# Kernel tuning notes

Hardware: AMD Instinct MI355X
Metric: run time of the kernel (lower is better)

Reference implementation:

```python
import jax, jax.numpy as jnp
import numpy as np

EPS_MASK = 1e-9   # module fills masked scores with eps, NOT -inf
LN_EPS = 1e-5

def _layer_norm(x, g, b):
    mu = jnp.mean(x, axis=-1, keepdims=True)
    var = jnp.mean(jnp.square(x - mu), axis=-1, keepdims=True)
    return (x - mu) * jax.lax.rsqrt(var + LN_EPS) * g + b

def _mha(q_in, k_in, v_in, wq, bq, wk, bk, wv, bv, wo, bo, mask, nhead):
    B, Sq, D = q_in.shape
    dk = D // nhead
    def proj(x, w, b):
        y = x @ w + b                                   # [B,S,D]
        return y.reshape(B, -1, nhead, dk).transpose(0, 2, 1, 3)  # [B,h,S,dk]
    q, k, v = proj(q_in, wq, bq), proj(k_in, wk, bk), proj(v_in, wv, bv)
    scores = jnp.einsum('bhqd,bhkd->bhqk', q, k) / np.sqrt(dk).astype(q.dtype)
    if mask is not None:
        scores = jnp.where(mask[:, None, :, :] == 0, jnp.asarray(EPS_MASK, scores.dtype), scores)
    p = jax.nn.softmax(scores, axis=-1)                 # dropout = identity (eval)
    x = jnp.einsum('bhqk,bhkd->bhqd', p, v)
    x = x.transpose(0, 2, 1, 3).reshape(B, Sq, D)
    return x @ wo + bo

def _forward_post(tgt, memory, tgt_pos, memory_pos, tgt_mask, memory_mask, p):
    nhead = 8
    # self-attention (q=k=tgt+pos, v=tgt)
    q = tgt + tgt_pos
    sa = _mha(q, q, tgt, p['sa_wq'], p['sa_bq'], p['sa_wk'], p['sa_bk'],
              p['sa_wv'], p['sa_bv'], p['sa_wo'], p['sa_bo'], tgt_mask, nhead)
    tgt = _layer_norm(tgt + sa, p['ln1_g'], p['ln1_b'])
    # cross-attention (q=tgt+tgt_pos, k=memory+memory_pos, v=memory)
    mq = tgt + tgt_pos
    mk = memory + memory_pos
    ca = _mha(mq, mk, memory, p['ca_wq'], p['ca_bq'], p['ca_wk'], p['ca_bk'],
              p['ca_wv'], p['ca_bv'], p['ca_wo'], p['ca_bo'], memory_mask, nhead)
    tgt = _layer_norm(tgt + ca, p['ln2_g'], p['ln2_b'])
    # FFN
    h = jax.nn.relu(tgt @ p['mlp_w1'] + p['mlp_b1'])
    ff = h @ p['mlp_w2'] + p['mlp_b2']
    return _layer_norm(tgt + ff, p['ln3_g'], p['ln3_b'])

def setup_inputs() -> dict:
    key = jax.random.key(0)
    B, S, M, D, H = 4, 1024, 1024, 512, 2048
    ks = iter(jax.random.split(key, 40))
    d = {
        'tgt': jax.random.normal(next(ks), (B, S, D), jnp.float32),
        'memory': jax.random.normal(next(ks), (B, M, D), jnp.float32),
        'tgt_pos': jax.random.normal(next(ks), (B, S, D), jnp.float32),
        'memory_pos': jax.random.normal(next(ks), (B, M, D), jnp.float32),
        'tgt_mask': jax.random.randint(next(ks), (B, S, S), 0, 2, jnp.int32),
        'memory_mask': jax.random.randint(next(ks), (B, S, M), 0, 2, jnp.int32),
    }
    for pre in ('sa', 'ca'):
        for nm in ('q', 'k', 'v', 'o'):
            d[f'{pre}_w{nm}'] = jax.random.normal(next(ks), (D, D), jnp.float32) * 0.02
            d[f'{pre}_b{nm}'] = jnp.zeros((D,), jnp.float32)
    for i in (1, 2, 3):
        d[f'ln{i}_g'] = jnp.ones((D,), jnp.float32)
        d[f'ln{i}_b'] = jnp.zeros((D,), jnp.float32)
    d['mlp_w1'] = jax.random.normal(next(ks), (D, H), jnp.float32) * 0.02
    d['mlp_b1'] = jnp.zeros((H,), jnp.float32)
    d['mlp_w2'] = jax.random.normal(next(ks), (H, D), jnp.float32) * 0.02
    d['mlp_b2'] = jnp.zeros((D,), jnp.float32)
    return d

def reference(tgt, memory, tgt_pos, memory_pos, tgt_mask, memory_mask,
              sa_wq, sa_bq, sa_wk, sa_bk, sa_wv, sa_bv, sa_wo, sa_bo,
              ca_wq, ca_bq, ca_wk, ca_bk, ca_wv, ca_bv, ca_wo, ca_bo,
              ln1_g, ln1_b, ln2_g, ln2_b, ln3_g, ln3_b,
              mlp_w1, mlp_b1, mlp_w2, mlp_b2):
    p = dict(sa_wq=sa_wq, sa_bq=sa_bq, sa_wk=sa_wk, sa_bk=sa_bk, sa_wv=sa_wv,
             sa_bv=sa_bv, sa_wo=sa_wo, sa_bo=sa_bo, ca_wq=ca_wq, ca_bq=ca_bq,
             ca_wk=ca_wk, ca_bk=ca_bk, ca_wv=ca_wv, ca_bv=ca_bv, ca_wo=ca_wo,
             ca_bo=ca_bo, ln1_g=ln1_g, ln1_b=ln1_b, ln2_g=ln2_g, ln2_b=ln2_b,
             ln3_g=ln3_g, ln3_b=ln3_b, mlp_w1=mlp_w1, mlp_b1=mlp_b1,
             mlp_w2=mlp_w2, mlp_b2=mlp_b2)
    return _forward_post(tgt, memory, tgt_pos, memory_pos, tgt_mask, memory_mask, p)
```

## Files before the change

kernel.cpp:

```cpp
#include <hip/hip_runtime.h>
#include <stdint.h>

typedef unsigned int u32;
typedef unsigned long long u64;
typedef unsigned short u16;
typedef __attribute__((ext_vector_type(8))) __bf16 bf16x8;
typedef __attribute__((ext_vector_type(4))) float f32x4;

#define DEV __device__ __forceinline__

DEV u16 f2bf(float f) {
    u32 x = __builtin_bit_cast(u32, f);
    u32 r = (x + 0x7FFFu + ((x >> 16) & 1u)) >> 16;
    return (u16)r;
}

DEV float bf2f(u16 x) {
    u32 u = (u32)x << 16;
    return __builtin_bit_cast(float, u);
}

DEV bf16x8 ldg8(const u16* p) {
    return __builtin_bit_cast(bf16x8, *(const uint4*)p);
}

DEV u32 pk2(float a, float b) {
    return (u32)f2bf(a) | ((u32)f2bf(b) << 16);
}

DEV void g2l16(const u16* g, u16* l) {
    __builtin_amdgcn_global_load_lds(
        (const __attribute__((address_space(1))) u32*)g,
        (__attribute__((address_space(3))) u32*)l, 16, 0, 0);
}

DEV f32x4 mfma16(bf16x8 a, bf16x8 b, f32x4 c) {
    return __builtin_amdgcn_mfma_f32_16x16x32_bf16(a, b, c, 0, 0, 0);
}

__global__ __launch_bounds__(256) void packmask_kernel(
    const int4* __restrict__ m1, const int4* __restrict__ m2,
    u32* __restrict__ o1, u32* __restrict__ o2, int n8) {
    int i = blockIdx.x * 256 + threadIdx.x;
    bool first = i < n8;
    int idx = first ? i : i - n8;
    const int4* src = first ? m1 : m2;
    int4 a = src[idx * 2], b = src[idx * 2 + 1];
    u32 by = (u32)(a.x != 0) | ((u32)(a.y != 0) << 1) | ((u32)(a.z != 0) << 2) |
             ((u32)(a.w != 0) << 3) | ((u32)(b.x != 0) << 4) | ((u32)(b.y != 0) << 5) |
             ((u32)(b.z != 0) << 6) | ((u32)(b.w != 0) << 7);
    u32 w = by | (__shfl_down(by, 1) << 8) | (__shfl_down(by, 2) << 16) |
            (__shfl_down(by, 3) << 24);
    if ((threadIdx.x & 3) == 0) (first ? o1 : o2)[idx >> 2] = w;
}

__global__ __launch_bounds__(256) void prep_kernel(
    const float4* __restrict__ tgt, const float4* __restrict__ tpos,
    const float4* __restrict__ mem, const float4* __restrict__ mpos,
    ushort4* __restrict__ qin, ushort4* __restrict__ tgtb,
    ushort4* __restrict__ memb, ushort4* __restrict__ mkb, int n4) {
    int i = blockIdx.x * 256 + threadIdx.x;
    if (i >= n4) return;
    float4 t = tgt[i], p = tpos[i], m = mem[i], mp = mpos[i];
    qin[i]  = make_ushort4(f2bf(t.x + p.x), f2bf(t.y + p.y), f2bf(t.z + p.z), f2bf(t.w + p.w));
    tgtb[i] = make_ushort4(f2bf(t.x), f2bf(t.y), f2bf(t.z), f2bf(t.w));
    memb[i] = make_ushort4(f2bf(m.x), f2bf(m.y), f2bf(m.z), f2bf(m.w));
    mkb[i]  = make_ushort4(f2bf(m.x + mp.x), f2bf(m.y + mp.y), f2bf(m.z + mp.z), f2bf(m.w + mp.w));
}

struct W10 { const float* w[10]; };
__global__ __launch_bounds__(256) void wtrans_kernel(W10 ws, u16* wtbase) {
    int z = blockIdx.y;
    int Kd = (z == 9) ? 2048 : 512;
    int Nd = (z == 8) ? 2048 : 512;
    size_t off = (z < 8) ? (size_t)z * 262144
                         : (z == 8 ? (size_t)2097152 : (size_t)3145728);
    u16* out = wtbase + off;
    int nx = Nd / 32;
    int txile = blockIdx.x % nx, tyile = blockIdx.x / nx;
    if (tyile >= Kd / 32) return;
    const float* w = ws.w[z];
    __shared__ float t[32][33];
    int tx = threadIdx.x, ty = threadIdx.y;
#pragma unroll
    for (int j = 0; j < 4; ++j)
        t[ty + j * 8][tx] = w[(size_t)(tyile * 32 + ty + j * 8) * Nd + txile * 32 + tx];
    __syncthreads();
#pragma unroll
    for (int j = 0; j < 4; ++j)
        out[(size_t)(txile * 32 + ty + j * 8) * Kd + tyile * 32 + tx] = f2bf(t[tx][ty + j * 8]);
}

struct GemmSet { const u16* A; const u16* W; const float* bias; void* out; float oscale; int epi; };
struct GemmArgs3 { GemmSet s[3]; };

template <int BM, int BN>
__global__ __launch_bounds__(256) void gemm_kernel(GemmArgs3 args, int M, int N, int Kd) {
    constexpr int MF = BM / 32, NF = BN / 32;
    const GemmSet gs = args.s[blockIdx.z];
    const u16* __restrict__ A = gs.A;
    const u16* __restrict__ W = gs.W;
    const int t = threadIdx.x;
    const int lane = t & 63;
    const int g = lane >> 4, r16 = lane & 15;
    const int wave = t >> 6;
    const int wm = wave >> 1, wn = wave & 1;
    const int nwg = gridDim.x * gridDim.y;
    const int fid = blockIdx.y * gridDim.x + blockIdx.x;
    const int qq = nwg >> 3;
    const int lid = (fid & 7) * qq + (fid >> 3);
    const int m0 = (lid / gridDim.x) * BM, n0 = (lid % gridDim.x) * BN;

    __shared__ __align__(16) u16 As[BM * 64];
    __shared__ __align__(16) u16 Bs[BN * 64];

    f32x4 acc[MF][NF];
#pragma unroll
    for (int m = 0; m < MF; ++m)
#pragma unroll
        for (int n = 0; n < NF; ++n) acc[m][n] = f32x4{0.f, 0.f, 0.f, 0.f};

    for (int kk = 0; kk < Kd; kk += 64) {
        __syncthreads();
#pragma unroll
        for (int i = 0; i < BM / 32; ++i) {
            int cid = t + i * 256, row = cid >> 3, c = cid & 7;
            g2l16(A + (size_t)(m0 + row) * Kd + kk + ((c ^ (row & 7)) << 3), &As[cid << 3]);
        }
#pragma unroll
        for (int i = 0; i < BN / 32; ++i) {
            int cid = t + i * 256, row = cid >> 3, c = cid & 7;
            g2l16(W + (size_t)(n0 + row) * Kd + kk + ((c ^ (row & 7)) << 3), &Bs[cid << 3]);
        }
        __syncthreads();
#pragma unroll
        for (int ks = 0; ks < 2; ++ks) {
            bf16x8 af[MF], bfr[NF];
#pragma unroll
            for (int m = 0; m < MF; ++m) {
                int row = wm * (MF * 16) + m * 16 + r16;
                af[m] = *(const bf16x8*)&As[(row << 6) + (((ks * 4 + g) ^ (row & 7)) << 3)];
            }
#pragma unroll
            for (int n = 0; n < NF; ++n) {
                int row = wn * (NF * 16) + n * 16 + r16;
                bfr[n] = *(const bf16x8*)&Bs[(row << 6) + (((ks * 4 + g) ^ (row & 7)) << 3)];
            }
#pragma unroll
            for (int m = 0; m < MF; ++m)
#pragma unroll
                for (int n = 0; n < NF; ++n)
                    acc[m][n] = mfma16(af[m], bfr[n], acc[m][n]);
        }
    }
    const int epi = gs.epi;
#pragma unroll
    for (int m = 0; m < MF; ++m) {
        int row0 = m0 + wm * (MF * 16) + m * 16 + g * 4;
#pragma unroll
        for (int n = 0; n < NF; ++n) {
            int col = n0 + wn * (NF * 16) + n * 16 + r16;
            float bv = gs.bias[col];
            float v[4];
#pragma unroll
            for (int r = 0; r < 4; ++r) v[r] = (acc[m][n][r] + bv) * gs.oscale;
            if (epi == 1) {
#pragma unroll
                for (int r = 0; r < 4; ++r) v[r] = fmaxf(v[r], 0.f);
            }
            if (epi == 2) {
                float* o = (float*)gs.out;
#pragma unroll
                for (int r = 0; r < 4; ++r) o[(size_t)(row0 + r) * N + col] = v[r];
            } else if (epi == 3) {
                int bb = row0 >> 10, s = row0 & 1023;
                u16* o = (u16*)gs.out +
                         ((size_t)(bb * 8 + (col >> 6)) * 64 + (col & 63)) * 1024 + s;
                *(ushort4*)o = make_ushort4(f2bf(v[0]), f2bf(v[1]), f2bf(v[2]), f2bf(v[3]));
            } else {
                u16* o = (u16*)gs.out;
#pragma unroll
                for (int r = 0; r < 4; ++r) o[(size_t)(row0 + r) * N + col] = f2bf(v[r]);
            }
        }
    }
}

__global__ __launch_bounds__(512) void attn_part_kernel(
    const u16* __restrict__ Q, const u16* __restrict__ K,
    const u16* __restrict__ VT, const u32* __restrict__ mb,
    u16* __restrict__ OP, float2* __restrict__ ML, int Lq, int Lk) {
    const int t = threadIdx.x, lane = t & 63, wave = t >> 6;
    const int g = lane >> 4, r16 = lane & 15;
    const int h = blockIdx.y;
    const int b = blockIdx.z >> 2, p = blockIdx.z & 3;
    const int bh = b * 8 + h;
    const int q0 = blockIdx.x * 128 + wave * 16;
    const int kc0 = p * (Lk >> 2);
    const int NCH = (Lk >> 2) >> 5;

    __shared__ __align__(16) u16 Ks[2][32][64];
    __shared__ __align__(16) u16 Vs[2][64][32];
    __shared__ __align__(16) u16 Pl[8][16][40];

    const size_t qrow = (size_t)b * Lq + q0 + r16;
    const u16* qp = Q + qrow * 512 + h * 64 + g * 8;
    bf16x8 qb0 = ldg8(qp), qb1 = ldg8(qp + 32);
    const u32* mrow = mb + qrow * (Lk >> 5);

    const int sid = t & 255;
    const bool isK = t < 256;
    const int srow = sid >> 3, sc = sid & 7;
    const int vd = sid >> 2, vc = sid & 3;
    const u16* sg = isK
        ? K + (size_t)b * Lk * 512 + h * 64 + (size_t)srow * 512 + ((sc ^ (srow & 7)) << 3)
        : VT + ((size_t)bh * 64 + vd) * Lk + (vc << 3);
    u16* const sl = (isK ? &Ks[0][0][0] : &Vs[0][0][0]) + sid * 8;
    const size_t sstride = isK ? 512 : 1;

    f32x4 acc[4];
#pragma unroll
    for (int dt = 0; dt < 4; ++dt) acc[dt] = f32x4{0.f, 0.f, 0.f, 0.f};
    float mrun = -INFINITY, lrun = 0.f;
    const f32x4 zf = {0.f, 0.f, 0.f, 0.f};

    g2l16(sg + (size_t)kc0 * sstride, sl);
    __syncthreads();

    for (int c = 0; c < NCH; ++c) {
        const int buf = c & 1, nbuf = buf ^ 1;
        const int kc = kc0 + c * 32;
        if (c + 1 < NCH)
            g2l16(sg + (size_t)(kc + 32) * sstride, sl + nbuf * 2048);
        const u16* kb = &Ks[buf][0][0];
        const u16* vb = &Vs[buf][0][0];
        const int r1 = 16 + r16;
        bf16x8 k00 = *(const bf16x8*)(kb + r16 * 64 + ((g ^ (r16 & 7)) << 3));
        bf16x8 k01 = *(const bf16x8*)(kb + r16 * 64 + (((4 + g) ^ (r16 & 7)) << 3));
        bf16x8 k10 = *(const bf16x8*)(kb + r1 * 64 + ((g ^ (r16 & 7)) << 3));
        bf16x8 k11 = *(const bf16x8*)(kb + r1 * 64 + (((4 + g) ^ (r16 & 7)) << 3));
        f32x4 s0 = mfma16(k00, qb0, zf); s0 = mfma16(k01, qb1, s0);
        f32x4 s1 = mfma16(k10, qb0, zf); s1 = mfma16(k11, qb1, s1);

        u32 mw = mrow[kc >> 5];
        float sv[8];
#pragma unroll
        for (int r = 0; r < 4; ++r) {
            sv[r]     = ((mw >> (g * 4 + r)) & 1) ? s0[r] : 1e-9f;
            sv[4 + r] = ((mw >> (16 + g * 4 + r)) & 1) ? s1[r] : 1e-9f;
        }
        float tm = fmaxf(fmaxf(fmaxf(sv[0], sv[1]), fmaxf(sv[2], sv[3])),
                         fmaxf(fmaxf(sv[4], sv[5]), fmaxf(sv[6], sv[7])));
        tm = fmaxf(tm, __shfl_xor(tm, 16));
        tm = fmaxf(tm, __shfl_xor(tm, 32));
        if (!__all(tm <= mrun + 8.f)) {
            float mn = fmaxf(mrun, tm);
            float alpha = __expf(mrun - mn);
            mrun = mn;
            lrun *= alpha;
#pragma unroll
            for (int r = 0; r < 4; ++r) {
                float ar = __shfl(alpha, g * 4 + r);
#pragma unroll
                for (int dt = 0; dt < 4; ++dt) acc[dt][r] *= ar;
            }
        }
        float ts = 0.f;
#pragma unroll
        for (int j = 0; j < 8; ++j) { sv[j] = __expf(sv[j] - mrun); ts += sv[j]; }
        ts += __shfl_xor(ts, 16);
        ts += __shfl_xor(ts, 32);
        lrun += ts;

        uint2 u0; u0.x = pk2(sv[0], sv[1]); u0.y = pk2(sv[2], sv[3]);
        uint2 u1; u1.x = pk2(sv[4], sv[5]); u1.y = pk2(sv[6], sv[7]);
        *(uint2*)&Pl[wave][r16][g * 4] = u0;
        *(uint2*)&Pl[wave][r16][16 + g * 4] = u1;
        bf16x8 pf = *(const bf16x8*)&Pl[wave][r16][g * 8];
#pragma unroll
        for (int dt = 0; dt < 4; ++dt) {
            bf16x8 vf = *(const bf16x8*)(vb + (dt * 16 + r16) * 32 + g * 8);
            acc[dt] = mfma16(pf, vf, acc[dt]);
        }
        __syncthreads();
    }

    if (lane < 16)
        ML[(size_t)p * 32768 + (size_t)bh * 1024 + q0 + lane] = make_float2(mrun, lrun);
    const size_t obase = (size_t)p * 2097152 + ((size_t)bh * 1024 + q0) * 64;
#pragma unroll
    for (int dt = 0; dt < 4; ++dt)
#pragma unroll
        for (int r = 0; r < 4; ++r)
            OP[obase + (size_t)(g * 4 + r) * 64 + dt * 16 + r16] = f2bf(acc[dt][r]);
}

__global__ __launch_bounds__(256) void attn_combine_kernel(
    const u16* __restrict__ OP, const float2* __restrict__ ML, u16* __restrict__ O) {
    int idx = blockIdx.x * 256 + threadIdx.x;
    int row = idx >> 6, d = idx & 63;
    float2 ml0 = ML[row], ml1 = ML[32768 + row];
    float2 ml2 = ML[65536 + row], ml3 = ML[98304 + row];
    float M = fmaxf(fmaxf(ml0.x, ml1.x), fmaxf(ml2.x, ml3.x));
    float w0 = __expf(ml0.x - M), w1 = __expf(ml1.x - M);
    float w2 = __expf(ml2.x - M), w3 = __expf(ml3.x - M);
    float den = ml0.y * w0 + ml1.y * w1 + ml2.y * w2 + ml3.y * w3;
    float v = (bf2f(OP[idx]) * w0 + bf2f(OP[2097152 + idx]) * w1 +
               bf2f(OP[4194304 + idx]) * w2 + bf2f(OP[6291456 + idx]) * w3) / den;
    int bh = row >> 10, q = row & 1023;
    int b = bh >> 3, h = bh & 7;
    O[((size_t)(b * 1024 + q)) * 512 + h * 64 + d] = f2bf(v);
}

template <int MODE>
__global__ __launch_bounds__(256) void ln_kernel(
    const float* __restrict__ a, const float* __restrict__ bsrc,
    const float* __restrict__ gam, const float* __restrict__ bet,
    const float* __restrict__ pos,
    float* __restrict__ yf, u16* __restrict__ yb, u16* __restrict__ qb) {
    const int lane = threadIdx.x & 63;
    const int row = blockIdx.x * 4 + (threadIdx.x >> 6);
    const size_t base = (size_t)row * 512 + lane * 8;
    float4 av0 = ((const float4*)(a + base))[0];
    float4 av1 = ((const float4*)(a + base))[1];
    float4 bv0 = ((const float4*)(bsrc + base))[0];
    float4 bv1 = ((const float4*)(bsrc + base))[1];
    float x[8] = {av0.x + bv0.x, av0.y + bv0.y, av0.z + bv0.z, av0.w + bv0.w,
                  av1.x + bv1.x, av1.y + bv1.y, av1.z + bv1.z, av1.w + bv1.w};
    float s1 = 0.f, s2 = 0.f;
#pragma unroll
    for (int j = 0; j < 8; ++j) { s1 += x[j]; s2 += x[j] * x[j]; }
#pragma unroll
    for (int d = 1; d < 64; d <<= 1) { s1 += __shfl_xor(s1, d); s2 += __shfl_xor(s2, d); }
    float mean = s1 * (1.f / 512.f);
    float var = s2 * (1.f / 512.f) - mean * mean;
    float rs = rsqrtf(var + 1e-5f);
    float4 gv0 = ((const float4*)(gam + lane * 8))[0];
    float4 gv1 = ((const float4*)(gam + lane * 8))[1];
    float4 be0 = ((const float4*)(bet + lane * 8))[0];
    float4 be1 = ((const float4*)(bet + lane * 8))[1];
    float gg[8] = {gv0.x, gv0.y, gv0.z, gv0.w, gv1.x, gv1.y, gv1.z, gv1.w};
    float bb[8] = {be0.x, be0.y, be0.z, be0.w, be1.x, be1.y, be1.z, be1.w};
    float y[8];
#pragma unroll
    for (int j = 0; j < 8; ++j) y[j] = (x[j] - mean) * rs * gg[j] + bb[j];
    ((float4*)(yf + base))[0] = make_float4(y[0], y[1], y[2], y[3]);
    ((float4*)(yf + base))[1] = make_float4(y[4], y[5], y[6], y[7]);
    if (MODE <= 1) {
        ((ushort4*)(yb + base))[0] = make_ushort4(f2bf(y[0]), f2bf(y[1]), f2bf(y[2]), f2bf(y[3]));
        ((ushort4*)(yb + base))[1] = make_ushort4(f2bf(y[4]), f2bf(y[5]), f2bf(y[6]), f2bf(y[7]));
    }
    if (MODE == 0) {
        float4 p0 = ((const float4*)(pos + base))[0];
        float4 p1 = ((const float4*)(pos + base))[1];
        ((ushort4*)(qb + base))[0] = make_ushort4(f2bf(y[0] + p0.x), f2bf(y[1] + p0.y),
                                                  f2bf(y[2] + p0.z), f2bf(y[3] + p0.w));
        ((ushort4*)(qb + base))[1] = make_ushort4(f2bf(y[4] + p1.x), f2bf(y[5] + p1.y),
                                                  f2bf(y[6] + p1.z), f2bf(y[7] + p1.w));
    }
}

extern "C" void kernel_launch(void* const* d_in, const int* in_sizes, int n_in,
                              void* d_out, int out_size, void* d_ws, size_t ws_size,
                              hipStream_t stream) {
    (void)in_sizes; (void)n_in; (void)out_size; (void)ws_size;
    const float* tgt      = (const float*)d_in[0];
    const float* memory   = (const float*)d_in[1];
    const float* tgt_pos  = (const float*)d_in[2];
    const float* mem_pos  = (const float*)d_in[3];
    const int*   tgt_mask = (const int*)d_in[4];
    const int*   mem_mask = (const int*)d_in[5];
    const float* sa_b[4] = {(const float*)d_in[7], (const float*)d_in[9],
                            (const float*)d_in[11], (const float*)d_in[13]};
    const float* ca_b[4] = {(const float*)d_in[15], (const float*)d_in[17],
                            (const float*)d_in[19], (const float*)d_in[21]};
    const float* ln1_g = (const float*)d_in[22]; const float* ln1_b = (const float*)d_in[23];
    const float* ln2_g = (const float*)d_in[24]; const float* ln2_b = (const float*)d_in[25];
    const float* ln3_g = (const float*)d_in[26]; const float* ln3_b = (const float*)d_in[27];
    const float* mlp_b1 = (const float*)d_in[29];
    const float* mlp_b2 = (const float*)d_in[31];

    const size_t MiB = 1024 * 1024;
    char* ws = (char*)d_ws;
    u16*  WT  = (u16*)(ws + 0);
    u32*  MBS = (u32*)(ws + 8 * MiB);
    u32*  MBC = (u32*)(ws + 8 * MiB + 512 * 1024);
    u16*  QIN = (u16*)(ws + 9 * MiB);
    u16*  TGTB= (u16*)(ws + 13 * MiB);
    u16*  MEMB= (u16*)(ws + 17 * MiB);
    u16*  MKB = (u16*)(ws + 21 * MiB);
    u16*  QM  = (u16*)(ws + 25 * MiB);
    u16*  KM  = (u16*)(ws + 29 * MiB);
    u16*  VTM = (u16*)(ws + 37 * MiB);
    u16*  ATNB= (u16*)(ws + 41 * MiB);
    float* PROJ= (float*)(ws + 45 * MiB);
    float* X1F = (float*)(ws + 53 * MiB);
    u16*  X1B = (u16*)(ws + 61 * MiB);
    u16*  MQB = (u16*)(ws + 65 * MiB);
    float* X2F = (float*)(ws + 69 * MiB);
    u16*  X2B = (u16*)(ws + 77 * MiB);
    u16*  FFH = (u16*)(ws + 9 * MiB);
    u16*  OPB = (u16*)(ws + 96 * MiB);
    float2* MLB = (float2*)(ws + 120 * MiB);

    u16* wt[10];
    for (int z = 0; z < 8; ++z) wt[z] = WT + (size_t)z * 262144;
    wt[8] = WT + 2097152;
    wt[9] = WT + 3145728;

    W10 w10;
    w10.w[0] = (const float*)d_in[6];  w10.w[1] = (const float*)d_in[8];
    w10.w[2] = (const float*)d_in[10]; w10.w[3] = (const float*)d_in[12];
    w10.w[4] = (const float*)d_in[14]; w10.w[5] = (const float*)d_in[16];
    w10.w[6] = (const float*)d_in[18]; w10.w[7] = (const float*)d_in[20];
    w10.w[8] = (const float*)d_in[28]; w10.w[9] = (const float*)d_in[30];
    wtrans_kernel<<<dim3(1024, 10), dim3(32, 8), 0, stream>>>(w10, WT);

    packmask_kernel<<<4096, 256, 0, stream>>>(
        (const int4*)tgt_mask, (const int4*)mem_mask, MBS, MBC, 524288);

    prep_kernel<<<2048, 256, 0, stream>>>(
        (const float4*)tgt, (const float4*)tgt_pos, (const float4*)memory, (const float4*)mem_pos,
        (ushort4*)QIN, (ushort4*)TGTB, (ushort4*)MEMB, (ushort4*)MKB, 524288);

    GemmArgs3 ga;
    ga.s[0] = {QIN,  wt[0], sa_b[0], QM,  0.125f, 0};
    ga.s[1] = {QIN,  wt[1], sa_b[1], KM,  1.f,    0};
    ga.s[2] = {TGTB, wt[2], sa_b[2], VTM, 1.f,    3};
    gemm_kernel<128, 64><<<dim3(8, 32, 3), 256, 0, stream>>>(ga, 4096, 512, 512);
    attn_part_kernel<<<dim3(8, 8, 16), 512, 0, stream>>>(QM, KM, VTM, MBS, OPB, MLB, 1024, 1024);
    attn_combine_kernel<<<8192, 256, 0, stream>>>(OPB, MLB, ATNB);
    ga.s[0] = {ATNB, wt[3], sa_b[3], PROJ, 1.f, 2}; ga.s[1] = ga.s[0]; ga.s[2] = ga.s[0];
    gemm_kernel<64, 64><<<dim3(8, 64, 1), 256, 0, stream>>>(ga, 4096, 512, 512);
    ln_kernel<0><<<1024, 256, 0, stream>>>(tgt, PROJ, ln1_g, ln1_b, tgt_pos, X1F, X1B, MQB);

    ga.s[0] = {MQB,  wt[4], ca_b[0], QM,  0.125f, 0};
    ga.s[1] = {MKB,  wt[5], ca_b[1], KM,  1.f,    0};
    ga.s[2] = {MEMB, wt[6], ca_b[2], VTM, 1.f,    3};
    gemm_kernel<128, 64><<<dim3(8, 32, 3), 256, 0, stream>>>(ga, 4096, 512, 512);
    attn_part_kernel<<<dim3(8, 8, 16), 512, 0, stream>>>(QM, KM, VTM, MBC, OPB, MLB, 1024, 1024);
    attn_combine_kernel<<<8192, 256, 0, stream>>>(OPB, MLB, ATNB);
    ga.s[0] = {ATNB, wt[7], ca_b[3], PROJ, 1.f, 2}; ga.s[1] = ga.s[0]; ga.s[2] = ga.s[0];
    gemm_kernel<64, 64><<<dim3(8, 64, 1), 256, 0, stream>>>(ga, 4096, 512, 512);
    ln_kernel<1><<<1024, 256, 0, stream>>>(X1F, PROJ, ln2_g, ln2_b, nullptr, X2F, X2B, nullptr);

    ga.s[0] = {X2B, wt[8], mlp_b1, FFH, 1.f, 1}; ga.s[1] = ga.s[0]; ga.s[2] = ga.s[0];
    gemm_kernel<128, 64><<<dim3(32, 32, 1), 256, 0, stream>>>(ga, 4096, 2048, 512);
    ga.s[0] = {FFH, wt[9], mlp_b2, PROJ, 1.f, 2}; ga.s[1] = ga.s[0]; ga.s[2] = ga.s[0];
    gemm_kernel<64, 64><<<dim3(8, 64, 1), 256, 0, stream>>>(ga, 4096, 512, 2048);
    ln_kernel<2><<<1024, 256, 0, stream>>>(X2F, PROJ, ln3_g, ln3_b, nullptr,
                                           (float*)d_out, nullptr, nullptr);
}
```

Before: 195.6 us.

## Merge prologue kernels, halve attention key splits, drop unused LN bf16 output

```diff
diff --git a/kernel.cpp b/kernel.cpp
--- a/kernel.cpp
+++ b/kernel.cpp
@@ -38,57 +38,57 @@
     return __builtin_amdgcn_mfma_f32_16x16x32_bf16(a, b, c, 0, 0, 0);
 }
 
-__global__ __launch_bounds__(256) void packmask_kernel(
-    const int4* __restrict__ m1, const int4* __restrict__ m2,
-    u32* __restrict__ o1, u32* __restrict__ o2, int n8) {
-    int i = blockIdx.x * 256 + threadIdx.x;
-    bool first = i < n8;
-    int idx = first ? i : i - n8;
-    const int4* src = first ? m1 : m2;
-    int4 a = src[idx * 2], b = src[idx * 2 + 1];
-    u32 by = (u32)(a.x != 0) | ((u32)(a.y != 0) << 1) | ((u32)(a.z != 0) << 2) |
-             ((u32)(a.w != 0) << 3) | ((u32)(b.x != 0) << 4) | ((u32)(b.y != 0) << 5) |
-             ((u32)(b.z != 0) << 6) | ((u32)(b.w != 0) << 7);
-    u32 w = by | (__shfl_down(by, 1) << 8) | (__shfl_down(by, 2) << 16) |
-            (__shfl_down(by, 3) << 24);
-    if ((threadIdx.x & 3) == 0) (first ? o1 : o2)[idx >> 2] = w;
-}
-
-__global__ __launch_bounds__(256) void prep_kernel(
-    const float4* __restrict__ tgt, const float4* __restrict__ tpos,
-    const float4* __restrict__ mem, const float4* __restrict__ mpos,
-    ushort4* __restrict__ qin, ushort4* __restrict__ tgtb,
-    ushort4* __restrict__ memb, ushort4* __restrict__ mkb, int n4) {
-    int i = blockIdx.x * 256 + threadIdx.x;
-    if (i >= n4) return;
-    float4 t = tgt[i], p = tpos[i], m = mem[i], mp = mpos[i];
-    qin[i]  = make_ushort4(f2bf(t.x + p.x), f2bf(t.y + p.y), f2bf(t.z + p.z), f2bf(t.w + p.w));
-    tgtb[i] = make_ushort4(f2bf(t.x), f2bf(t.y), f2bf(t.z), f2bf(t.w));
-    memb[i] = make_ushort4(f2bf(m.x), f2bf(m.y), f2bf(m.z), f2bf(m.w));
-    mkb[i]  = make_ushort4(f2bf(m.x + mp.x), f2bf(m.y + mp.y), f2bf(m.z + mp.z), f2bf(m.w + mp.w));
-}
-
-struct W10 { const float* w[10]; };
-__global__ __launch_bounds__(256) void wtrans_kernel(W10 ws, u16* wtbase) {
-    int z = blockIdx.y;
-    int Kd = (z == 9) ? 2048 : 512;
-    int Nd = (z == 8) ? 2048 : 512;
-    size_t off = (z < 8) ? (size_t)z * 262144
-                         : (z == 8 ? (size_t)2097152 : (size_t)3145728);
-    u16* out = wtbase + off;
-    int nx = Nd / 32;
-    int txile = blockIdx.x % nx, tyile = blockIdx.x / nx;
-    if (tyile >= Kd / 32) return;
-    const float* w = ws.w[z];
-    __shared__ float t[32][33];
-    int tx = threadIdx.x, ty = threadIdx.y;
-#pragma unroll
-    for (int j = 0; j < 4; ++j)
-        t[ty + j * 8][tx] = w[(size_t)(tyile * 32 + ty + j * 8) * Nd + txile * 32 + tx];
-    __syncthreads();
-#pragma unroll
-    for (int j = 0; j < 4; ++j)
-        out[(size_t)(txile * 32 + ty + j * 8) * Kd + tyile * 32 + tx] = f2bf(t[tx][ty + j * 8]);
+struct ProArgs {
+    const float* w[10];
+    u16* wtbase;
+    const float4 *tgt, *tpos, *mem, *mpos;
+    ushort4 *qin, *tgtb, *memb, *mkb;
+    const int4 *m1, *m2;
+    u32 *o1, *o2;
+};
+__global__ __launch_bounds__(256) void prologue_kernel(ProArgs a) {
+    const int bx = blockIdx.x, t = threadIdx.x;
+    if (bx < 10240) {
+        int z = bx >> 10, bxx = bx & 1023;
+        int Kd = (z == 9) ? 2048 : 512;
+        int Nd = (z == 8) ? 2048 : 512;
+        size_t off = (z < 8) ? (size_t)z * 262144
+                             : (z == 8 ? (size_t)2097152 : (size_t)3145728);
+        u16* out = a.wtbase + off;
+        int nx = Nd / 32;
+        int txile = bxx % nx, tyile = bxx / nx;
+        if (tyile >= Kd / 32) return;
+        const float* w = a.w[z];
+        __shared__ float tl[32][33];
+        int tx = t & 31, ty = t >> 5;
+#pragma unroll
+        for (int j = 0; j < 4; ++j)
+            tl[ty + j * 8][tx] = w[(size_t)(tyile * 32 + ty + j * 8) * Nd + txile * 32 + tx];
+        __syncthreads();
+#pragma unroll
+        for (int j = 0; j < 4; ++j)
+            out[(size_t)(txile * 32 + ty + j * 8) * Kd + tyile * 32 + tx] = f2bf(tl[tx][ty + j * 8]);
+    } else if (bx < 12288) {
+        int i = (bx - 10240) * 256 + t;
+        float4 tt = a.tgt[i], p = a.tpos[i], m = a.mem[i], mp = a.mpos[i];
+        a.qin[i]  = make_ushort4(f2bf(tt.x + p.x), f2bf(tt.y + p.y), f2bf(tt.z + p.z), f2bf(tt.w + p.w));
+        a.tgtb[i] = make_ushort4(f2bf(tt.x), f2bf(tt.y), f2bf(tt.z), f2bf(tt.w));
+        a.memb[i] = make_ushort4(f2bf(m.x), f2bf(m.y), f2bf(m.z), f2bf(m.w));
+        a.mkb[i]  = make_ushort4(f2bf(m.x + mp.x), f2bf(m.y + mp.y), f2bf(m.z + mp.z), f2bf(m.w + mp.w));
+    } else {
+        int i = (bx - 12288) * 256 + t;
+        const int n8 = 524288;
+        bool first = i < n8;
+        int idx = first ? i : i - n8;
+        const int4* src = first ? a.m1 : a.m2;
+        int4 x = src[idx * 2], y = src[idx * 2 + 1];
+        u32 by = (u32)(x.x != 0) | ((u32)(x.y != 0) << 1) | ((u32)(x.z != 0) << 2) |
+                 ((u32)(x.w != 0) << 3) | ((u32)(y.x != 0) << 4) | ((u32)(y.y != 0) << 5) |
+                 ((u32)(y.z != 0) << 6) | ((u32)(y.w != 0) << 7);
+        u32 w = by | (__shfl_down(by, 1) << 8) | (__shfl_down(by, 2) << 16) |
+                (__shfl_down(by, 3) << 24);
+        if ((t & 3) == 0) (first ? a.o1 : a.o2)[idx >> 2] = w;
+    }
 }
 
 struct GemmSet { const u16* A; const u16* W; const float* bias; void* out; float oscale; int epi; };
@@ -193,11 +193,11 @@
     const int t = threadIdx.x, lane = t & 63, wave = t >> 6;
     const int g = lane >> 4, r16 = lane & 15;
     const int h = blockIdx.y;
-    const int b = blockIdx.z >> 2, p = blockIdx.z & 3;
+    const int b = blockIdx.z >> 1, p = blockIdx.z & 1;
     const int bh = b * 8 + h;
     const int q0 = blockIdx.x * 128 + wave * 16;
-    const int kc0 = p * (Lk >> 2);
-    const int NCH = (Lk >> 2) >> 5;
+    const int kc0 = p * (Lk >> 1);
+    const int NCH = (Lk >> 1) >> 5;
 
     __shared__ __align__(16) u16 Ks[2][32][64];
     __shared__ __align__(16) u16 Vs[2][64][32];
@@ -300,13 +300,10 @@
     int idx = blockIdx.x * 256 + threadIdx.x;
     int row = idx >> 6, d = idx & 63;
     float2 ml0 = ML[row], ml1 = ML[32768 + row];
-    float2 ml2 = ML[65536 + row], ml3 = ML[98304 + row];
-    float M = fmaxf(fmaxf(ml0.x, ml1.x), fmaxf(ml2.x, ml3.x));
+    float M = fmaxf(ml0.x, ml1.x);
     float w0 = __expf(ml0.x - M), w1 = __expf(ml1.x - M);
-    float w2 = __expf(ml2.x - M), w3 = __expf(ml3.x - M);
-    float den = ml0.y * w0 + ml1.y * w1 + ml2.y * w2 + ml3.y * w3;
-    float v = (bf2f(OP[idx]) * w0 + bf2f(OP[2097152 + idx]) * w1 +
-               bf2f(OP[4194304 + idx]) * w2 + bf2f(OP[6291456 + idx]) * w3) / den;
+    float den = ml0.y * w0 + ml1.y * w1;
+    float v = (bf2f(OP[idx]) * w0 + bf2f(OP[2097152 + idx]) * w1) / den;
     int bh = row >> 10, q = row & 1023;
     int b = bh >> 3, h = bh & 7;
     O[((size_t)(b * 1024 + q)) * 512 + h * 64 + d] = f2bf(v);
@@ -346,7 +343,7 @@
     for (int j = 0; j < 8; ++j) y[j] = (x[j] - mean) * rs * gg[j] + bb[j];
     ((float4*)(yf + base))[0] = make_float4(y[0], y[1], y[2], y[3]);
     ((float4*)(yf + base))[1] = make_float4(y[4], y[5], y[6], y[7]);
-    if (MODE <= 1) {
+    if (MODE == 1) {
         ((ushort4*)(yb + base))[0] = make_ushort4(f2bf(y[0]), f2bf(y[1]), f2bf(y[2]), f2bf(y[3]));
         ((ushort4*)(yb + base))[1] = make_ushort4(f2bf(y[4]), f2bf(y[5]), f2bf(y[6]), f2bf(y[7]));
     }
@@ -395,7 +392,6 @@
     u16*  ATNB= (u16*)(ws + 41 * MiB);
     float* PROJ= (float*)(ws + 45 * MiB);
     float* X1F = (float*)(ws + 53 * MiB);
-    u16*  X1B = (u16*)(ws + 61 * MiB);
     u16*  MQB = (u16*)(ws + 65 * MiB);
     float* X2F = (float*)(ws + 69 * MiB);
     u16*  X2B = (u16*)(ws + 77 * MiB);
@@ -408,37 +404,37 @@
     wt[8] = WT + 2097152;
     wt[9] = WT + 3145728;
 
-    W10 w10;
-    w10.w[0] = (const float*)d_in[6];  w10.w[1] = (const float*)d_in[8];
-    w10.w[2] = (const float*)d_in[10]; w10.w[3] = (const float*)d_in[12];
-    w10.w[4] = (const float*)d_in[14]; w10.w[5] = (const float*)d_in[16];
-    w10.w[6] = (const float*)d_in[18]; w10.w[7] = (const float*)d_in[20];
-    w10.w[8] = (const float*)d_in[28]; w10.w[9] = (const float*)d_in[30];
-    wtrans_kernel<<<dim3(1024, 10), dim3(32, 8), 0, stream>>>(w10, WT);
-
-    packmask_kernel<<<4096, 256, 0, stream>>>(
-        (const int4*)tgt_mask, (const int4*)mem_mask, MBS, MBC, 524288);
-
-    prep_kernel<<<2048, 256, 0, stream>>>(
-        (const float4*)tgt, (const float4*)tgt_pos, (const float4*)memory, (const float4*)mem_pos,
-        (ushort4*)QIN, (ushort4*)TGTB, (ushort4*)MEMB, (ushort4*)MKB, 524288);
+    ProArgs pa;
+    pa.w[0] = (const float*)d_in[6];  pa.w[1] = (const float*)d_in[8];
+    pa.w[2] = (const float*)d_in[10]; pa.w[3] = (const float*)d_in[12];
+    pa.w[4] = (const float*)d_in[14]; pa.w[5] = (const float*)d_in[16];
+    pa.w[6] = (const float*)d_in[18]; pa.w[7] = (const float*)d_in[20];
+    pa.w[8] = (const float*)d_in[28]; pa.w[9] = (const float*)d_in[30];
+    pa.wtbase = WT;
+    pa.tgt = (const float4*)tgt; pa.tpos = (const float4*)tgt_pos;
+    pa.mem = (const float4*)memory; pa.mpos = (const float4*)mem_pos;
+    pa.qin = (ushort4*)QIN; pa.tgtb = (ushort4*)TGTB;
+    pa.memb = (ushort4*)MEMB; pa.mkb = (ushort4*)MKB;
+    pa.m1 = (const int4*)tgt_mask; pa.m2 = (const int4*)mem_mask;
+    pa.o1 = MBS; pa.o2 = MBC;
+    prologue_kernel<<<16384, 256, 0, stream>>>(pa);
 
     GemmArgs3 ga;
     ga.s[0] = {QIN,  wt[0], sa_b[0], QM,  0.125f, 0};
     ga.s[1] = {QIN,  wt[1], sa_b[1], KM,  1.f,    0};
     ga.s[2] = {TGTB, wt[2], sa_b[2], VTM, 1.f,    3};
     gemm_kernel<128, 64><<<dim3(8, 32, 3), 256, 0, stream>>>(ga, 4096, 512, 512);
-    attn_part_kernel<<<dim3(8, 8, 16), 512, 0, stream>>>(QM, KM, VTM, MBS, OPB, MLB, 1024, 1024);
+    attn_part_kernel<<<dim3(8, 8, 8), 512, 0, stream>>>(QM, KM, VTM, MBS, OPB, MLB, 1024, 1024);
     attn_combine_kernel<<<8192, 256, 0, stream>>>(OPB, MLB, ATNB);
     ga.s[0] = {ATNB, wt[3], sa_b[3], PROJ, 1.f, 2}; ga.s[1] = ga.s[0]; ga.s[2] = ga.s[0];
     gemm_kernel<64, 64><<<dim3(8, 64, 1), 256, 0, stream>>>(ga, 4096, 512, 512);
-    ln_kernel<0><<<1024, 256, 0, stream>>>(tgt, PROJ, ln1_g, ln1_b, tgt_pos, X1F, X1B, MQB);
+    ln_kernel<0><<<1024, 256, 0, stream>>>(tgt, PROJ, ln1_g, ln1_b, tgt_pos, X1F, nullptr, MQB);
 
     ga.s[0] = {MQB,  wt[4], ca_b[0], QM,  0.125f, 0};
     ga.s[1] = {MKB,  wt[5], ca_b[1], KM,  1.f,    0};
     ga.s[2] = {MEMB, wt[6], ca_b[2], VTM, 1.f,    3};
     gemm_kernel<128, 64><<<dim3(8, 32, 3), 256, 0, stream>>>(ga, 4096, 512, 512);
-    attn_part_kernel<<<dim3(8, 8, 16), 512, 0, stream>>>(QM, KM, VTM, MBC, OPB, MLB, 1024, 1024);
+    attn_part_kernel<<<dim3(8, 8, 8), 512, 0, stream>>>(QM, KM, VTM, MBC, OPB, MLB, 1024, 1024);
     attn_combine_kernel<<<8192, 256, 0, stream>>>(OPB, MLB, ATNB);
     ga.s[0] = {ATNB, wt[7], ca_b[3], PROJ, 1.f, 2}; ga.s[1] = ga.s[0]; ga.s[2] = ga.s[0];
     gemm_kernel<64, 64><<<dim3(8, 64, 1), 256, 0, stream>>>(ga, 4096, 512, 512);
```

New measurement: 184.8 us. 5.6% less time.
